# Optimization experiments

Hardware: AMD Instinct MI355X
Metric: run time of the kernel (lower is better)

Reference implementation:

```python
import jax, jax.numpy as jnp
import numpy as np

NUM_HEADS = 3

def setup_inputs() -> dict:
    key = jax.random.key(0)
    k0, k1, k2, k3, k4 = jax.random.split(key, 5)
    B, C, H, W = 2, 96, 64, 64
    N = H * W
    x = jax.random.normal(k0, (B, N, C), jnp.float32)
    # depthwise conv: groups=C, out_channels=3*C -> OIHW weight [3C, 1, 3, 3]
    qkv_w = jax.random.normal(k1, (3 * C, 1, 3, 3), jnp.float32) * 0.1
    qkv_b = jax.random.normal(k2, (3 * C,), jnp.float32) * 0.01
    proj_w = jax.random.normal(k3, (C, C), jnp.float32) * (1.0 / np.sqrt(C))
    proj_b = jax.random.normal(k4, (C,), jnp.float32) * 0.01
    return {"x": x, "qkv_w": qkv_w, "qkv_b": qkv_b,
            "proj_w": proj_w, "proj_b": proj_b, "H": H, "W": W}


def reference(x, qkv_w, qkv_b, proj_w, proj_b, H, W):
    B, N, C = x.shape
    h = NUM_HEADS
    d = C // h
    scale = d ** (-0.5)
    # [B,N,C] -> [B,C,H,W]
    x2d = jnp.transpose(x, (0, 2, 1)).reshape(B, C, H, W)
    # depthwise conv, 'SAME' padding (padding = kernel//2, stride 1)
    qkv = jax.lax.conv_general_dilated(
        x2d, qkv_w, window_strides=(1, 1), padding="SAME",
        feature_group_count=C,
        dimension_numbers=("NCHW", "OIHW", "NCHW"))
    qkv = qkv + qkv_b[None, :, None, None]
    qkv = qkv.reshape(B, 3, h, d, H * W)  # same channel split as torch reshape
    q, k, v = qkv[:, 0], qkv[:, 1], qkv[:, 2]  # each [B,h,d,N]
    # attn = q^T @ k  (q,k permuted to [B,h,N,d] in the original)
    attn = jnp.einsum("bhdn,bhdm->bhnm", q, k) * scale  # [B,h,N,N]
    attn = jax.nn.softmax(attn, axis=-1)
    out = jnp.einsum("bhnm,bhdm->bhnd", attn, v)  # [B,h,N,d]
    # replicate torch: transpose(2,3) -> [B,h,d,N], reshape(B, N, C)
    out = jnp.transpose(out, (0, 1, 3, 2)).reshape(B, H * W, C)
    out = out @ proj_w.T + proj_b
    return out
```

## Files before the change

kernel.cpp:

```cpp
#include <hip/hip_runtime.h>
#include <hip/hip_bf16.h>

typedef short bf16x8 __attribute__((ext_vector_type(8)));
typedef float f32x4 __attribute__((ext_vector_type(4)));
typedef unsigned int u32x2 __attribute__((ext_vector_type(2)));

#define B_ 2
#define C_ 96
#define N_ 4096
#define NH_ 3
#define DH_ 32
#define BH_ 6
#define KSPLIT 2
#define TQ 32
#define TK 64
#define WAVES_PER_BLOCK 4
#define KT_PER_WAVE (N_ / KSPLIT / WAVES_PER_BLOCK / TK)


__global__ __launch_bounds__(256) void conv_qkv(
    const float* __restrict__ x, const float* __restrict__ qw,
    const float* __restrict__ qb, __hip_bfloat16* __restrict__ q_b,
    __hip_bfloat16* __restrict__ k_b, __hip_bfloat16* __restrict__ vT) {
  __shared__ float xs[18 * 64];
  int b = blockIdx.x / C_;
  int cin = blockIdx.x % C_;
  int y0 = blockIdx.y * 16;
  int yl0 = (y0 == 0) ? 0 : y0 - 1;
  int yl1 = (y0 + 16 > 63) ? 63 : y0 + 16;
  int nload = (yl1 - yl0 + 1) * 64;
  const float* xp = x + (size_t)b * N_ * C_ + cin;
  for (int i = threadIdx.x; i < nload; i += 256)
    xs[i] = xp[(size_t)(yl0 * 64 + i) * C_];
  __syncthreads();

  int s = cin >> 5;
  int cl = cin & 31;
  float w[3][9], bias[3];
#pragma unroll
  for (int r = 0; r < 3; ++r) {
    int o = 3 * cin + r;
#pragma unroll
    for (int t = 0; t < 9; ++t) w[r][t] = qw[o * 9 + t];
    bias[r] = qb[o];
  }
  const float scale = 0.2550349f;
  float mul = (s == 0) ? scale : 1.0f;
  __hip_bfloat16* base_[3];
  int dd_[3];
#pragma unroll
  for (int r = 0; r < 3; ++r) {
    int c = 3 * cl + r, head = c >> 5, dd = c & 31, bh = b * NH_ + head;
    dd_[r] = dd;
    if (s == 2)
      base_[r] = vT + (size_t)bh * N_ * DH_;
    else if (s == 1)
      base_[r] = k_b + (size_t)bh * N_ * DH_;
    else
      base_[r] = q_b + (size_t)bh * N_ * DH_;
  }

  for (int i = threadIdx.x; i < 1024; i += 256) {
    int y = y0 + (i >> 6), xx = i & 63;
    float a0 = bias[0], a1 = bias[1], a2 = bias[2];
#pragma unroll
    for (int dy = 0; dy < 3; ++dy) {
      int ry = y + dy - 1;
      if ((unsigned)ry >= 64u) continue;
#pragma unroll
      for (int dx = 0; dx < 3; ++dx) {
        int rx = xx + dx - 1;
        if ((unsigned)rx >= 64u) continue;
        float xv = xs[(ry - yl0) * 64 + rx];
        a0 += w[0][dy * 3 + dx] * xv;
        a1 += w[1][dy * 3 + dx] * xv;
        a2 += w[2][dy * 3 + dx] * xv;
      }
    }
    int n = y * 64 + xx;
    float av[3] = {a0 * mul, a1 * mul, a2 * mul};
#pragma unroll
    for (int r = 0; r < 3; ++r) {
      int off;
      if (s == 0)
        off = n * DH_ + dd_[r];
      else if (s == 1)
        off = ((n >> 6) << 11) | ((n & 3) << 9) | (((n >> 2) & 15) << 5) | dd_[r];
      else
        off = ((n >> 6) << 11) | (((n >> 5) & 1) << 10) | (dd_[r] << 5) | (n & 31);
      base_[r][off] = __float2bfloat16(av[r]);
    }
  }
}

__global__ __launch_bounds__(256, 2) void attn_fwd(
    const __hip_bfloat16* __restrict__ q_b, const __hip_bfloat16* __restrict__ k_b,
    const __hip_bfloat16* __restrict__ vT, float* __restrict__ Opart,
    float* __restrict__ lpart) {
  __shared__ __align__(16) unsigned char smemP[WAVES_PER_BLOCK][4608];
  __shared__ float l_s[WAVES_PER_BLOCK][32];
  int qt = blockIdx.x, ks = blockIdx.y, bh = blockIdx.z;
  int tid = threadIdx.x;
  int lane = tid & 63, wave = tid >> 6;
  int c = lane & 15, quad = lane >> 4;
  __hip_bfloat16* Pw = (__hip_bfloat16*)smemP[wave];

  const __hip_bfloat16* qbase = q_b + ((size_t)bh * N_ + qt * TQ) * DH_;
  bf16x8 qa[2];
#pragma unroll
  for (int m = 0; m < 2; ++m)
    qa[m] = *(const bf16x8*)(qbase + (m * 16 + c) * DH_ + quad * 8);

  f32x4 o[2][2];
  f32x4 lac[2];
#pragma unroll
  for (int m = 0; m < 2; ++m) {
    lac[m] = (f32x4){0.f, 0.f, 0.f, 0.f};
#pragma unroll
    for (int n0 = 0; n0 < 2; ++n0) o[m][n0] = (f32x4){0.f, 0.f, 0.f, 0.f};
  }
  bf16x8 ones;
  {
    short v = (c == 0) ? (short)0x3F80 : (short)0;
    ones = (bf16x8){v, v, v, v, v, v, v, v};
  }

  const __hip_bfloat16* kb = k_b + (size_t)bh * N_ * DH_;
  const __hip_bfloat16* vb = vT + (size_t)bh * N_ * DH_;
  int key0 = ks * (N_ / KSPLIT) + wave * (N_ / KSPLIT / WAVES_PER_BLOCK);

  bf16x8 kf[2][4];
  {
    size_t tb0 = (size_t)key0 * DH_;
#pragma unroll
    for (int t = 0; t < 4; ++t)
      kf[0][t] = *(const bf16x8*)(kb + tb0 + t * 512 + c * 32 + quad * 8);
  }

#pragma unroll
  for (int kt = 0; kt < KT_PER_WAVE; ++kt) {
    const int cur = kt & 1, nxt = cur ^ 1;
    size_t tbase = (size_t)(key0 + kt * TK) * DH_;

    if (kt + 1 < KT_PER_WAVE) {
      size_t tnext = (size_t)(key0 + (kt + 1) * TK) * DH_;
#pragma unroll
      for (int t = 0; t < 4; ++t)
        kf[nxt][t] = *(const bf16x8*)(kb + tnext + t * 512 + c * 32 + quad * 8);
    }

    f32x4 p[2][4];
    f32x4 z = {0.f, 0.f, 0.f, 0.f};
#pragma unroll
    for (int m = 0; m < 2; ++m)
#pragma unroll
      for (int t = 0; t < 4; ++t)
        p[m][t] = __builtin_amdgcn_mfma_f32_16x16x32_bf16(qa[m], kf[cur][t], z, 0, 0, 0);

    bf16x8 vf[2][2];
#pragma unroll
    for (int n0 = 0; n0 < 2; ++n0)
#pragma unroll
      for (int h = 0; h < 2; ++h)
        vf[n0][h] = *(const bf16x8*)(vb + tbase + h * 1024 + (n0 * 16 + c) * 32 + quad * 8);

#pragma unroll
    for (int m = 0; m < 2; ++m)
#pragma unroll
      for (int t = 0; t < 4; ++t)
#pragma unroll
        for (int r = 0; r < 4; ++r)
          p[m][t][r] = __builtin_amdgcn_exp2f(p[m][t][r]);

#pragma unroll
    for (int m = 0; m < 2; ++m)
#pragma unroll
      for (int r = 0; r < 4; ++r) {
        unsigned short h0 = __builtin_bit_cast(unsigned short, __float2bfloat16(p[m][0][r]));
        unsigned short h1 = __builtin_bit_cast(unsigned short, __float2bfloat16(p[m][1][r]));
        unsigned short h2 = __builtin_bit_cast(unsigned short, __float2bfloat16(p[m][2][r]));
        unsigned short h3 = __builtin_bit_cast(unsigned short, __float2bfloat16(p[m][3][r]));
        u32x2 pk;
        pk[0] = (unsigned)h0 | ((unsigned)h1 << 16);
        pk[1] = (unsigned)h2 | ((unsigned)h3 << 16);
        int row = m * 16 + quad * 4 + r;
        *(u32x2*)(Pw + row * 72 + 4 * c) = pk;
      }

    bf16x8 pA[2][2];
#pragma unroll
    for (int m = 0; m < 2; ++m)
#pragma unroll
      for (int h = 0; h < 2; ++h)
        pA[m][h] = *(const bf16x8*)(Pw + (m * 16 + c) * 72 + h * 32 + quad * 8);

#pragma unroll
    for (int m = 0; m < 2; ++m) {
#pragma unroll
      for (int n0 = 0; n0 < 2; ++n0) {
        o[m][n0] = __builtin_amdgcn_mfma_f32_16x16x32_bf16(pA[m][0], vf[n0][0], o[m][n0], 0, 0, 0);
        o[m][n0] = __builtin_amdgcn_mfma_f32_16x16x32_bf16(pA[m][1], vf[n0][1], o[m][n0], 0, 0, 0);
      }
      lac[m] = __builtin_amdgcn_mfma_f32_16x16x32_bf16(pA[m][0], ones, lac[m], 0, 0, 0);
      lac[m] = __builtin_amdgcn_mfma_f32_16x16x32_bf16(pA[m][1], ones, lac[m], 0, 0, 0);
    }
  }

  float* T = (float*)smemP[wave];
#pragma unroll
  for (int m = 0; m < 2; ++m)
#pragma unroll
    for (int n0 = 0; n0 < 2; ++n0)
#pragma unroll
      for (int r = 0; r < 4; ++r)
        T[(n0 * 16 + c) * 33 + m * 16 + quad * 4 + r] = o[m][n0][r];
  if (c == 0) {
#pragma unroll
    for (int m = 0; m < 2; ++m)
#pragma unroll
      for (int r = 0; r < 4; ++r) l_s[wave][m * 16 + quad * 4 + r] = lac[m][r];
  }
  __syncthreads();

  int nbase = qt * TQ;
  float* Ob = Opart + (size_t)(ks * BH_ + bh) * DH_ * N_ + nbase;
  const float* Sf = (const float*)smemP;
#pragma unroll
  for (int it = 0; it < 4; ++it) {
    int idx = it * 256 + tid;
    int dd = idx >> 5, q = idx & 31;
    float s = Sf[0 * 1152 + dd * 33 + q] + Sf[1 * 1152 + dd * 33 + q] +
              Sf[2 * 1152 + dd * 33 + q] + Sf[3 * 1152 + dd * 33 + q];
    Ob[(size_t)dd * N_ + q] = s;
  }
  if (tid < 32) {
    float s = l_s[0][tid] + l_s[1][tid] + l_s[2][tid] + l_s[3][tid];
    lpart[(size_t)(ks * BH_ + bh) * N_ + nbase + tid] = s;
  }
}

__global__ __launch_bounds__(256) void proj_out(
    const float* __restrict__ Opart, const float* __restrict__ lpart,
    const float* __restrict__ pw, const float* __restrict__ pb,
    float* __restrict__ out) {
  __shared__ float Wt[C_][100];
  __shared__ float Pt[16][100];
  __shared__ float bias[C_];
  int tid = threadIdx.x;
  for (int i = tid; i < C_ * C_; i += 256) Wt[i / C_][i % C_] = pw[i];
  if (tid < C_) bias[tid] = pb[tid];
  int row0 = blockIdx.x * 16;
  for (int i = tid; i < 16 * C_; i += 256) {
    int r = i / C_, cc = i % C_;
    int g = row0 + r;
    int b = g >> 12;
    int f = (g & 4095) * C_ + cc;
    int hh = f >> 17;
    int n = f & 4095;
    float osum = 0.f, lsum = 0.f;
    size_t obase = (size_t)g * C_ + cc;
    size_t lbase = (size_t)(b * NH_ + hh) * N_ + n;
#pragma unroll
    for (int ksq = 0; ksq < KSPLIT; ++ksq) {
      osum += Opart[(size_t)ksq * (BH_ * DH_ * N_) + obase];
      lsum += lpart[(size_t)ksq * (BH_ * N_) + lbase];
    }
    Pt[r][cc] = osum / lsum;
  }
  __syncthreads();

  int row = tid >> 4, cg = tid & 15;
  float acc[6] = {};
  for (int kk = 0; kk < C_; kk += 4) {
    f32x4 pv = *(const f32x4*)&Pt[row][kk];
    f32x4 wv[6];
#pragma unroll
    for (int i2 = 0; i2 < 6; ++i2) wv[i2] = *(const f32x4*)&Wt[cg * 6 + i2][kk];
#pragma unroll
    for (int i2 = 0; i2 < 6; ++i2)
      acc[i2] += pv[0] * wv[i2][0] + pv[1] * wv[i2][1] +
                 pv[2] * wv[i2][2] + pv[3] * wv[i2][3];
  }
#pragma unroll
  for (int i2 = 0; i2 < 6; ++i2)
    out[(size_t)(row0 + row) * C_ + cg * 6 + i2] = acc[i2] + bias[cg * 6 + i2];
}

extern "C" void kernel_launch(void* const* d_in, const int* in_sizes, int n_in,
                              void* d_out, int out_size, void* d_ws, size_t ws_size,
                              hipStream_t stream) {
  const float* x = (const float*)d_in[0];
  const float* qw = (const float*)d_in[1];
  const float* qb = (const float*)d_in[2];
  const float* pw = (const float*)d_in[3];
  const float* pb = (const float*)d_in[4];

  char* ws = (char*)d_ws;
  __hip_bfloat16* q_b = (__hip_bfloat16*)(ws);
  __hip_bfloat16* k_b = (__hip_bfloat16*)(ws + 1572864);
  __hip_bfloat16* vT = (__hip_bfloat16*)(ws + 3145728);
  float* Opart = (float*)(ws + 4718592);
  float* lpart = (float*)(ws + 11010048);

  hipLaunchKernelGGL(conv_qkv, dim3(B_ * C_, 4), dim3(256), 0, stream, x, qw, qb, q_b, k_b, vT);
  hipLaunchKernelGGL(attn_fwd, dim3(N_ / TQ, KSPLIT, BH_), dim3(256), 0, stream,
                     q_b, k_b, vT, Opart, lpart);
  hipLaunchKernelGGL(proj_out, dim3((B_ * N_) / 16, 1), dim3(256), 0, stream,
                     Opart, lpart, pw, pb, (float*)d_out);
}
```

Before: 125.0 us.

## Compute transposed scores so P stays in registers, removing LDS round-trip

Computes S^T = K·Q^T with the MFMA so the exp'd probabilities come out in the register layout the PV MFMA needs as its B operand, which removes the per-tile LDS store and reload of P. The K and V^T global layouts written by the conv kernel are permuted to match this new fragment mapping. The output and row-sum accumulators are now transposed, so the epilogue's shared-memory writeback indexing changes accordingly. This cuts LDS traffic and the wait between the two matmuls, at the cost of more intricate layout coupling between the two kernels.

```diff
diff --git a/kernel.cpp b/kernel.cpp
--- a/kernel.cpp
+++ b/kernel.cpp
@@ -3,7 +3,7 @@
 
 typedef short bf16x8 __attribute__((ext_vector_type(8)));
 typedef float f32x4 __attribute__((ext_vector_type(4)));
-typedef unsigned int u32x2 __attribute__((ext_vector_type(2)));
+typedef unsigned int u32x4 __attribute__((ext_vector_type(4)));
 
 #define B_ 2
 #define C_ 96
@@ -85,9 +85,11 @@
       if (s == 0)
         off = n * DH_ + dd_[r];
       else if (s == 1)
-        off = ((n >> 6) << 11) | ((n & 3) << 9) | (((n >> 2) & 15) << 5) | dd_[r];
-      else
-        off = ((n >> 6) << 11) | (((n >> 5) & 1) << 10) | (dd_[r] << 5) | (n & 31);
+        off = ((n >> 6) << 11) | (((n >> 4) & 3) << 9) | ((n & 15) << 5) | dd_[r];
+      else {
+        int kap = (((n >> 2) & 3) << 3) | (((n >> 4) & 1) << 2) | (n & 3);
+        off = ((n >> 6) << 11) | (((n >> 5) & 1) << 10) | (dd_[r] << 5) | kap;
+      }
       base_[r][off] = __float2bfloat16(av[r]);
     }
   }
@@ -97,13 +99,12 @@
     const __hip_bfloat16* __restrict__ q_b, const __hip_bfloat16* __restrict__ k_b,
     const __hip_bfloat16* __restrict__ vT, float* __restrict__ Opart,
     float* __restrict__ lpart) {
-  __shared__ __align__(16) unsigned char smemP[WAVES_PER_BLOCK][4608];
+  __shared__ __align__(16) float Tm[WAVES_PER_BLOCK][32 * 33];
   __shared__ float l_s[WAVES_PER_BLOCK][32];
   int qt = blockIdx.x, ks = blockIdx.y, bh = blockIdx.z;
   int tid = threadIdx.x;
   int lane = tid & 63, wave = tid >> 6;
   int c = lane & 15, quad = lane >> 4;
-  __hip_bfloat16* Pw = (__hip_bfloat16*)smemP[wave];
 
   const __hip_bfloat16* qbase = q_b + ((size_t)bh * N_ + qt * TQ) * DH_;
   bf16x8 qa[2];
@@ -111,13 +112,13 @@
   for (int m = 0; m < 2; ++m)
     qa[m] = *(const bf16x8*)(qbase + (m * 16 + c) * DH_ + quad * 8);
 
-  f32x4 o[2][2];
-  f32x4 lac[2];
+  f32x4 oT[2][2];
+  f32x4 lacT[2];
 #pragma unroll
   for (int m = 0; m < 2; ++m) {
-    lac[m] = (f32x4){0.f, 0.f, 0.f, 0.f};
-#pragma unroll
-    for (int n0 = 0; n0 < 2; ++n0) o[m][n0] = (f32x4){0.f, 0.f, 0.f, 0.f};
+    lacT[m] = (f32x4){0.f, 0.f, 0.f, 0.f};
+#pragma unroll
+    for (int n0 = 0; n0 < 2; ++n0) oT[n0][m] = (f32x4){0.f, 0.f, 0.f, 0.f};
   }
   bf16x8 ones;
   {
@@ -149,14 +150,6 @@
         kf[nxt][t] = *(const bf16x8*)(kb + tnext + t * 512 + c * 32 + quad * 8);
     }
 
-    f32x4 p[2][4];
-    f32x4 z = {0.f, 0.f, 0.f, 0.f};
-#pragma unroll
-    for (int m = 0; m < 2; ++m)
-#pragma unroll
-      for (int t = 0; t < 4; ++t)
-        p[m][t] = __builtin_amdgcn_mfma_f32_16x16x32_bf16(qa[m], kf[cur][t], z, 0, 0, 0);
-
     bf16x8 vf[2][2];
 #pragma unroll
     for (int n0 = 0; n0 < 2; ++n0)
@@ -165,72 +158,63 @@
         vf[n0][h] = *(const bf16x8*)(vb + tbase + h * 1024 + (n0 * 16 + c) * 32 + quad * 8);
 
 #pragma unroll
+    for (int m = 0; m < 2; ++m) {
+      f32x4 pT[4];
+      f32x4 z = {0.f, 0.f, 0.f, 0.f};
+#pragma unroll
+      for (int t = 0; t < 4; ++t)
+        pT[t] = __builtin_amdgcn_mfma_f32_16x16x32_bf16(kf[cur][t], qa[m], z, 0, 0, 0);
+
+#pragma unroll
+      for (int t = 0; t < 4; ++t)
+#pragma unroll
+        for (int r = 0; r < 4; ++r)
+          pT[t][r] = __builtin_amdgcn_exp2f(pT[t][r]);
+
+      unsigned wv[4][2];
+#pragma unroll
+      for (int t = 0; t < 4; ++t) {
+        unsigned h0 = __builtin_bit_cast(unsigned short, __float2bfloat16(pT[t][0]));
+        unsigned h1 = __builtin_bit_cast(unsigned short, __float2bfloat16(pT[t][1]));
+        unsigned h2 = __builtin_bit_cast(unsigned short, __float2bfloat16(pT[t][2]));
+        unsigned h3 = __builtin_bit_cast(unsigned short, __float2bfloat16(pT[t][3]));
+        wv[t][0] = h0 | (h1 << 16);
+        wv[t][1] = h2 | (h3 << 16);
+      }
+#pragma unroll
+      for (int h = 0; h < 2; ++h) {
+        u32x4 bw = {wv[2 * h][0], wv[2 * h][1], wv[2 * h + 1][0], wv[2 * h + 1][1]};
+        bf16x8 pB = __builtin_bit_cast(bf16x8, bw);
+        oT[0][m] = __builtin_amdgcn_mfma_f32_16x16x32_bf16(vf[0][h], pB, oT[0][m], 0, 0, 0);
+        oT[1][m] = __builtin_amdgcn_mfma_f32_16x16x32_bf16(vf[1][h], pB, oT[1][m], 0, 0, 0);
+        lacT[m] = __builtin_amdgcn_mfma_f32_16x16x32_bf16(ones, pB, lacT[m], 0, 0, 0);
+      }
+    }
+  }
+
+  float* T = Tm[wave];
+#pragma unroll
+  for (int n0 = 0; n0 < 2; ++n0)
+#pragma unroll
     for (int m = 0; m < 2; ++m)
 #pragma unroll
-      for (int t = 0; t < 4; ++t)
-#pragma unroll
-        for (int r = 0; r < 4; ++r)
-          p[m][t][r] = __builtin_amdgcn_exp2f(p[m][t][r]);
-
-#pragma unroll
-    for (int m = 0; m < 2; ++m)
-#pragma unroll
-      for (int r = 0; r < 4; ++r) {
-        unsigned short h0 = __builtin_bit_cast(unsigned short, __float2bfloat16(p[m][0][r]));
-        unsigned short h1 = __builtin_bit_cast(unsigned short, __float2bfloat16(p[m][1][r]));
-        unsigned short h2 = __builtin_bit_cast(unsigned short, __float2bfloat16(p[m][2][r]));
-        unsigned short h3 = __builtin_bit_cast(unsigned short, __float2bfloat16(p[m][3][r]));
-        u32x2 pk;
-        pk[0] = (unsigned)h0 | ((unsigned)h1 << 16);
-        pk[1] = (unsigned)h2 | ((unsigned)h3 << 16);
-        int row = m * 16 + quad * 4 + r;
-        *(u32x2*)(Pw + row * 72 + 4 * c) = pk;
-      }
-
-    bf16x8 pA[2][2];
-#pragma unroll
-    for (int m = 0; m < 2; ++m)
-#pragma unroll
-      for (int h = 0; h < 2; ++h)
-        pA[m][h] = *(const bf16x8*)(Pw + (m * 16 + c) * 72 + h * 32 + quad * 8);
-
-#pragma unroll
-    for (int m = 0; m < 2; ++m) {
-#pragma unroll
-      for (int n0 = 0; n0 < 2; ++n0) {
-        o[m][n0] = __builtin_amdgcn_mfma_f32_16x16x32_bf16(pA[m][0], vf[n0][0], o[m][n0], 0, 0, 0);
-        o[m][n0] = __builtin_amdgcn_mfma_f32_16x16x32_bf16(pA[m][1], vf[n0][1], o[m][n0], 0, 0, 0);
-      }
-      lac[m] = __builtin_amdgcn_mfma_f32_16x16x32_bf16(pA[m][0], ones, lac[m], 0, 0, 0);
-      lac[m] = __builtin_amdgcn_mfma_f32_16x16x32_bf16(pA[m][1], ones, lac[m], 0, 0, 0);
-    }
-  }
-
-  float* T = (float*)smemP[wave];
-#pragma unroll
-  for (int m = 0; m < 2; ++m)
-#pragma unroll
-    for (int n0 = 0; n0 < 2; ++n0)
-#pragma unroll
       for (int r = 0; r < 4; ++r)
-        T[(n0 * 16 + c) * 33 + m * 16 + quad * 4 + r] = o[m][n0][r];
-  if (c == 0) {
-#pragma unroll
-    for (int m = 0; m < 2; ++m)
-#pragma unroll
-      for (int r = 0; r < 4; ++r) l_s[wave][m * 16 + quad * 4 + r] = lac[m][r];
+        T[(n0 * 16 + quad * 4 + r) * 33 + m * 16 + c] = oT[n0][m][r];
+  if (lane < 16) {
+#pragma unroll
+    for (int m = 0; m < 2; ++m) l_s[wave][m * 16 + lane] = lacT[m][0];
   }
   __syncthreads();
 
   int nbase = qt * TQ;
   float* Ob = Opart + (size_t)(ks * BH_ + bh) * DH_ * N_ + nbase;
-  const float* Sf = (const float*)smemP;
+  const float* Sf = (const float*)Tm;
 #pragma unroll
   for (int it = 0; it < 4; ++it) {
     int idx = it * 256 + tid;
     int dd = idx >> 5, q = idx & 31;
-    float s = Sf[0 * 1152 + dd * 33 + q] + Sf[1 * 1152 + dd * 33 + q] +
-              Sf[2 * 1152 + dd * 33 + q] + Sf[3 * 1152 + dd * 33 + q];
+    float s = Sf[0 * 1056 + dd * 33 + q] + Sf[1 * 1056 + dd * 33 + q] +
+              Sf[2 * 1056 + dd * 33 + q] + Sf[3 * 1056 + dd * 33 + q];
     Ob[(size_t)dd * N_ + q] = s;
   }
   if (tid < 32) {
```

Measured after the change: 123.4 us. About the same (-1.3%).
